# Optimization experiments

Measured on AMD Instinct MI355X. Metric: run time of the kernel, lower is better.

## Reference

```python
import jax, jax.numpy as jnp
import numpy as np

N_NODES = 100000


def gcn_conv(x, src, dst, W, b, n_nodes):
    """PyG-style GCNConv: linear transform, symmetric-normalized aggregation with self loops."""
    h = x @ W  # (N, out)
    e = src.shape[0]
    # degree including the implicit self loop (edge weights = 1)
    deg = jax.ops.segment_sum(jnp.ones((e,), dtype=h.dtype), dst, num_segments=n_nodes) + 1.0
    dis = jax.lax.rsqrt(deg)  # deg^{-1/2}
    coef = dis[src] * dis[dst]  # (E,)
    msg = h[src] * coef[:, None]  # (E, out) -- gather + scale
    agg = jax.ops.segment_sum(msg, dst, num_segments=n_nodes)  # scatter-add
    agg = agg + h * (dis * dis)[:, None]  # self-loop contribution
    return agg + b


def setup_inputs() -> dict:
    key = jax.random.key(0)
    k = jax.random.split(key, 6)
    in_dim, hid, out = 128, 128, 64
    E = 1600000
    x = jax.random.normal(k[0], (N_NODES, in_dim), dtype=jnp.float32)
    edge_index = jax.random.randint(k[1], (2, E), 0, N_NODES, dtype=jnp.int64)
    W1 = jax.random.normal(k[2], (in_dim, hid), dtype=jnp.float32) * (1.0 / np.sqrt(in_dim))
    b1 = jnp.zeros((hid,), dtype=jnp.float32)
    W2 = jax.random.normal(k[3], (hid, out), dtype=jnp.float32) * (1.0 / np.sqrt(hid))
    b2 = jnp.zeros((out,), dtype=jnp.float32)
    return {"x": x, "edge_index": edge_index, "W1": W1, "b1": b1, "W2": W2, "b2": b2}


def reference(x, edge_index, W1, b1, W2, b2):
    src, dst = edge_index[0], edge_index[1]
    h = gcn_conv(x, src, dst, W1, b1, N_NODES)
    h = jax.nn.relu(h)
    # dropout is identity in eval mode
    h = gcn_conv(h, src, dst, W2, b2, N_NODES)
    # L2 normalize along feature dim (F.normalize, eps=1e-12)
    norm = jnp.maximum(jnp.linalg.norm(h, axis=-1, keepdims=True), 1e-12)
    return h / norm
```

## Files before the change

### kernel.cpp

```cpp
#include <hip/hip_runtime.h>
#include <hip/hip_bf16.h>
#include <math.h>

#define CSHIFT 9
#define TILE   4096
#define PSH    14

using f16x8 = __attribute__((ext_vector_type(8))) _Float16;
using f16x2 = __attribute__((ext_vector_type(2))) _Float16;
using f32x4 = __attribute__((ext_vector_type(4))) float;

__device__ __forceinline__ unsigned pack_f16(float lo, float hi) {
    auto h = __builtin_amdgcn_cvt_pkrtz(lo, hi);
    return *(unsigned*)&h;
}
__device__ __forceinline__ f16x2 h2(unsigned u) { return *(f16x2*)&u; }

__device__ __forceinline__ unsigned pack_fp8x4(float f0, float f1, float f2, float f3) {
    int w = 0;
    w = __builtin_amdgcn_cvt_pk_fp8_f32(f0, f1, w, false);
    w = __builtin_amdgcn_cvt_pk_fp8_f32(f2, f3, w, true);
    return (unsigned)w;
}
__device__ __forceinline__ void fp8x4_acc(unsigned v, float& a0, float& a1, float& a2, float& a3) {
    auto lo = __builtin_amdgcn_cvt_pk_f32_fp8((int)v, false);
    auto hi = __builtin_amdgcn_cvt_pk_f32_fp8((int)v, true);
    a0 += lo[0]; a1 += lo[1]; a2 += hi[0]; a3 += hi[1];
}

__global__ void k_prep(const float* __restrict__ W1, const float* __restrict__ W2,
                       unsigned short* __restrict__ wp1, unsigned short* __restrict__ wp2,
                       int* __restrict__ ccursor, unsigned* __restrict__ g1,
                       unsigned* __restrict__ g2, int NC, int N) {
    int idx = blockIdx.x * 256 + threadIdx.x;
    if (idx < NC) ccursor[idx] = idx << PSH;
    if (idx < 32) {
        g1[(size_t)N * 32 + idx] = 0u;
        g2[(size_t)N * 32 + idx] = 0u;
    }
    if (idx < 16384) {
        int e = idx & 7, l = (idx >> 3) & 63, f = idx >> 9;
        int nt = f & 7, kt = f >> 3;
        int k = kt * 32 + (l >> 4) * 8 + e, nn = nt * 16 + (l & 15);
        _Float16 hv = (_Float16)W1[k * 128 + nn];
        wp1[idx] = *(unsigned short*)&hv;
    }
    int i2 = idx - 16384;
    if (i2 >= 0 && i2 < 8192) {
        int e = i2 & 7, l = (i2 >> 3) & 63, f = i2 >> 9;
        int nt = f & 3, kt = f >> 2;
        int k = kt * 32 + (l >> 4) * 8 + e, nn = nt * 16 + (l & 15);
        _Float16 hv = (_Float16)W2[k * 64 + nn];
        wp2[i2] = *(unsigned short*)&hv;
    }
}

__global__ __launch_bounds__(256) void k_part(const int* __restrict__ src,
                                              const int* __restrict__ dst, int E,
                                              int* __restrict__ ccursor,
                                              int* __restrict__ pairs, int NC) {
    __shared__ int sdst[TILE];
    __shared__ int stg[TILE];
    __shared__ unsigned char sbk[TILE];
    __shared__ int h[256], delta[256], cur[256];
    __shared__ int sa[256], sb[256];
    int t = threadIdx.x;
    int base = blockIdx.x * TILE;
    int cnt = min(TILE, E - base);

    h[t] = 0; __syncthreads();
    #pragma unroll
    for (int k = 0; k < TILE / 256; ++k) {
        int e = base + k * 256 + t;
        int d = (e < E) ? dst[e] : -1;
        sdst[k * 256 + t] = d;
        if (d >= 0) atomicAdd(&h[d >> CSHIFT], 1);
    }
    __syncthreads();
    int myc = h[t];
    int* c_ = sa; int* n_ = sb;
    c_[t] = myc; __syncthreads();
    for (int o = 1; o < 256; o <<= 1) {
        int val = c_[t] + ((t >= o) ? c_[t - o] : 0);
        n_[t] = val; __syncthreads();
        int* tmp = c_; c_ = n_; n_ = tmp;
    }
    int ex = c_[t] - myc;
    cur[t] = ex;
    int g = 0;
    if (t < NC && myc) g = atomicAdd(&ccursor[t], myc);
    delta[t] = g - ex;
    __syncthreads();

    #pragma unroll
    for (int k = 0; k < TILE / 256; ++k) {
        int e = base + k * 256 + t;
        if (e < E) {
            int d = sdst[k * 256 + t];
            int b = d >> CSHIFT;
            int p = atomicAdd(&cur[b], 1);
            stg[p] = src[e] | ((d & 511) << 17);
            sbk[p] = (unsigned char)b;
        }
    }
    __syncthreads();
    for (int i = t; i < cnt; i += 256)
        pairs[delta[sbk[i]] + i] = stg[i];
}

__global__ __launch_bounds__(256) void k_build(const int* __restrict__ ccursor,
                                               const int* __restrict__ pairs,
                                               int2* __restrict__ seg,
                                               float* __restrict__ dis,
                                               int* __restrict__ csr, int N) {
    __shared__ int h[512];
    __shared__ int cur[512];
    __shared__ int sa[256], sb[256];
    int b = blockIdx.x, t = threadIdx.x;
    h[t] = 0; h[t + 256] = 0; __syncthreads();
    int beg = b << PSH, end = ccursor[b];
    for (int i = beg + t; i < end; i += 256) atomicAdd(&h[pairs[i] >> 17], 1);
    __syncthreads();
    int h0 = h[2 * t], h1 = h[2 * t + 1];
    int p0 = (h0 + 15) & ~15;
    int p1 = (h1 + 15) & ~15;
    int s = p0 + p1;
    int* c_ = sa; int* n_ = sb;
    c_[t] = s; __syncthreads();
    for (int o = 1; o < 256; o <<= 1) {
        int val = c_[t] + ((t >= o) ? c_[t - o] : 0);
        n_[t] = val; __syncthreads();
        int* tmp = c_; c_ = n_; n_ = tmp;
    }
    int ex = c_[t] - s;
    int d0 = b << CSHIFT;
    int da = d0 + 2 * t, db = da + 1;
    cur[2 * t] = ex; cur[2 * t + 1] = ex + p0;
    if (da < N) { seg[da] = make_int2(beg + ex, beg + ex + p0);       dis[da] = rsqrtf((float)h0 + 1.0f); }
    if (db < N) { seg[db] = make_int2(beg + ex + p0, beg + ex + p0 + p1); dis[db] = rsqrtf((float)h1 + 1.0f); }
    for (int i = h0; i < p0; ++i) csr[beg + ex + i] = N;
    for (int i = h1; i < p1; ++i) csr[beg + ex + p0 + i] = N;
    __syncthreads();
    for (int i = beg + t; i < end; i += 256) {
        int pk = pairs[i];
        int p = atomicAdd(&cur[pk >> 17], 1);
        csr[beg + p] = pk & 0x1FFFF;
    }
}

__global__ __launch_bounds__(256) void k_gemm1(
    const float* __restrict__ A, const unsigned short* __restrict__ wp,
    const float* __restrict__ dis, unsigned* __restrict__ G, int M)
{
    constexpr int NT = 8;
    constexpr int ND = 32;

    union UW { uint4 q; f16x8 v; };
    union UA { unsigned u[4]; f16x8 v; };

    const int tid  = threadIdx.x;
    const int wv   = tid >> 6;
    const int lane = tid & 63;
    const int lm   = lane & 15;
    const int lk   = lane >> 4;
    const int m0   = blockIdx.x * 128 + wv * 32;

    f16x8 xf[2][4];
    int mrow[2];
    #pragma unroll
    for (int mt = 0; mt < 2; ++mt) {
        int m = m0 + mt * 16 + lm;
        mrow[mt] = m;
        int mc = m < M ? m : (M - 1);
        const float* Ar = A + (size_t)mc * 128;
        #pragma unroll
        for (int kt = 0; kt < 4; ++kt) {
            int cb = kt * 32 + lk * 8;
            float4 p = *(const float4*)(Ar + cb);
            float4 q = *(const float4*)(Ar + cb + 4);
            UA u;
            u.u[0] = pack_f16(p.x, p.y);
            u.u[1] = pack_f16(p.z, p.w);
            u.u[2] = pack_f16(q.x, q.y);
            u.u[3] = pack_f16(q.z, q.w);
            xf[mt][kt] = u.v;
        }
    }

    f32x4 acc[2][NT];
    #pragma unroll
    for (int mt = 0; mt < 2; ++mt)
        #pragma unroll
        for (int nt = 0; nt < NT; ++nt)
            #pragma unroll
            for (int r = 0; r < 4; ++r) acc[mt][nt][r] = 0.f;

    const uint4* wpv = (const uint4*)wp;
    #pragma unroll
    for (int kt = 0; kt < 4; ++kt) {
        f16x8 wf[NT];
        #pragma unroll
        for (int nt = 0; nt < NT; ++nt) {
            UW u; u.q = wpv[(kt * NT + nt) * 64 + lane];
            wf[nt] = u.v;
        }
        #pragma unroll
        for (int mt = 0; mt < 2; ++mt)
            #pragma unroll
            for (int nt = 0; nt < NT; ++nt)
                acc[mt][nt] = __builtin_amdgcn_mfma_f32_16x16x32_f16(
                    wf[nt], xf[mt][kt], acc[mt][nt], 0, 0, 0);
    }

    #pragma unroll
    for (int mt = 0; mt < 2; ++mt) {
        int m = mrow[mt];
        if (m < M) {
            float dd = dis[m];
            unsigned* gr = G + (size_t)m * ND;
            #pragma unroll
            for (int nt = 0; nt < NT; ++nt)
                gr[nt * 4 + lk] = pack_fp8x4(acc[mt][nt][0] * dd, acc[mt][nt][1] * dd,
                                             acc[mt][nt][2] * dd, acc[mt][nt][3] * dd);
        }
    }
}

__global__ __launch_bounds__(256) void k_agg1(
    const unsigned* __restrict__ g1, const int2* __restrict__ seg,
    const int* __restrict__ csr, const float* __restrict__ dis,
    const float* __restrict__ b1, unsigned* __restrict__ y1, int n)
{
    int wid  = (blockIdx.x * 256 + threadIdx.x) >> 6;
    int lane = threadIdx.x & 63;
    if (wid >= n) return;
    int d  = wid;
    int ll = lane & 31;
    int eh = lane >> 5;
    int2 se = seg[d];
    int beg = se.x, pend = se.y;

    float a0 = 0.f, a1 = 0.f, a2 = 0.f, a3 = 0.f;
    if (eh == 0)
        fp8x4_acc(g1[(size_t)d * 32 + ll], a0, a1, a2, a3);

    for (int j = beg; j < pend; j += 16) {
        unsigned v[8];
        #pragma unroll
        for (int k = 0; k < 8; ++k)
            v[k] = g1[(size_t)csr[j + 2 * k + eh] * 32 + ll];
        #pragma unroll
        for (int k = 0; k < 8; ++k)
            fp8x4_acc(v[k], a0, a1, a2, a3);
    }

    a0 += __shfl_xor(a0, 32, 64);
    a1 += __shfl_xor(a1, 32, 64);
    a2 += __shfl_xor(a2, 32, 64);
    a3 += __shfl_xor(a3, 32, 64);

    float dd = dis[d];
    float4 bb = *(const float4*)(b1 + 4 * ll);
    float o0 = fmaxf(fmaf(dd, a0, bb.x), 0.f);
    float o1 = fmaxf(fmaf(dd, a1, bb.y), 0.f);
    float o2 = fmaxf(fmaf(dd, a2, bb.z), 0.f);
    float o3 = fmaxf(fmaf(dd, a3, bb.w), 0.f);
    if (lane < 32) {
        uint2 w;
        w.x = pack_f16(o0, o1);
        w.y = pack_f16(o2, o3);
        *((uint2*)(y1 + (size_t)d * 64) + ll) = w;
    }
}

__global__ __launch_bounds__(256) void k_gemm2(
    const unsigned short* __restrict__ A, const unsigned short* __restrict__ wp,
    const float* __restrict__ dis, unsigned* __restrict__ G, int M)
{
    constexpr int NT = 4;
    constexpr int ND = 32;
    union UW { uint4 q; f16x8 v; };

    const int tid  = threadIdx.x;
    const int wv   = tid >> 6;
    const int lane = tid & 63;
    const int lm   = lane & 15;
    const int lk   = lane >> 4;
    const int m0   = blockIdx.x * 128 + wv * 32;

    f16x8 xf[2][4];
    int mrow[2];
    #pragma unroll
    for (int mt = 0; mt < 2; ++mt) {
        int m = m0 + mt * 16 + lm;
        mrow[mt] = m;
        int mc = m < M ? m : (M - 1);
        const uint4* Ar = (const uint4*)(A + (size_t)mc * 128);
        #pragma unroll
        for (int kt = 0; kt < 4; ++kt) {
            UW u; u.q = Ar[kt * 4 + lk];
            xf[mt][kt] = u.v;
        }
    }

    f32x4 acc[2][NT];
    #pragma unroll
    for (int mt = 0; mt < 2; ++mt)
        #pragma unroll
        for (int nt = 0; nt < NT; ++nt)
            #pragma unroll
            for (int r = 0; r < 4; ++r) acc[mt][nt][r] = 0.f;

    const uint4* wpv = (const uint4*)wp;
    #pragma unroll
    for (int kt = 0; kt < 4; ++kt) {
        f16x8 wf[NT];
        #pragma unroll
        for (int nt = 0; nt < NT; ++nt) {
            UW u; u.q = wpv[(kt * NT + nt) * 64 + lane];
            wf[nt] = u.v;
        }
        #pragma unroll
        for (int mt = 0; mt < 2; ++mt)
            #pragma unroll
            for (int nt = 0; nt < NT; ++nt)
                acc[mt][nt] = __builtin_amdgcn_mfma_f32_16x16x32_f16(
                    wf[nt], xf[mt][kt], acc[mt][nt], 0, 0, 0);
    }

    #pragma unroll
    for (int mt = 0; mt < 2; ++mt) {
        int m = mrow[mt];
        if (m < M) {
            float dd = dis[m];
            unsigned* gr = G + (size_t)m * ND;
            #pragma unroll
            for (int nt = 0; nt < NT; ++nt) {
                uint2 w;
                w.x = pack_f16(acc[mt][nt][0] * dd, acc[mt][nt][1] * dd);
                w.y = pack_f16(acc[mt][nt][2] * dd, acc[mt][nt][3] * dd);
                *(uint2*)(gr + nt * 8 + lk * 2) = w;
            }
        }
    }
}

__global__ __launch_bounds__(256) void k_agg2(
    const unsigned* __restrict__ g2, const int2* __restrict__ seg,
    const int* __restrict__ csr, const float* __restrict__ dis,
    const float* __restrict__ b2, float* __restrict__ out, int n)
{
    int wid  = (blockIdx.x * 256 + threadIdx.x) >> 6;
    int lane = threadIdx.x & 63;
    if (wid >= n) return;
    int d  = wid;
    int ql = lane & 15;
    int qh = lane >> 4;
    int2 se = seg[d];
    int beg = se.x, pend = se.y;

    float a0 = 0.f, a1 = 0.f, a2 = 0.f, a3 = 0.f;
    int j = beg;
    for (; j + 32 <= pend; j += 32) {
        uint2 v[8];
        #pragma unroll
        for (int k = 0; k < 8; ++k) {
            int s = csr[j + 4 * k + qh];
            v[k] = *((const uint2*)(g2 + (size_t)s * 32) + ql);
        }
        #pragma unroll
        for (int k = 0; k < 8; k += 2) {
            f16x2 sx = h2(v[k].x) + h2(v[k + 1].x);
            f16x2 sy = h2(v[k].y) + h2(v[k + 1].y);
            a0 += (float)sx[0]; a1 += (float)sx[1];
            a2 += (float)sy[0]; a3 += (float)sy[1];
        }
    }
    if (j < pend) {
        uint2 v[4];
        #pragma unroll
        for (int k = 0; k < 4; ++k) {
            int s = csr[j + 4 * k + qh];
            v[k] = *((const uint2*)(g2 + (size_t)s * 32) + ql);
        }
        #pragma unroll
        for (int k = 0; k < 4; k += 2) {
            f16x2 sx = h2(v[k].x) + h2(v[k + 1].x);
            f16x2 sy = h2(v[k].y) + h2(v[k + 1].y);
            a0 += (float)sx[0]; a1 += (float)sx[1];
            a2 += (float)sy[0]; a3 += (float)sy[1];
        }
    }

    a0 += __shfl_xor(a0, 16, 64); a0 += __shfl_xor(a0, 32, 64);
    a1 += __shfl_xor(a1, 16, 64); a1 += __shfl_xor(a1, 32, 64);
    a2 += __shfl_xor(a2, 16, 64); a2 += __shfl_xor(a2, 32, 64);
    a3 += __shfl_xor(a3, 16, 64); a3 += __shfl_xor(a3, 32, 64);

    uint2 sv = *((const uint2*)(g2 + (size_t)d * 32) + ql);
    f16x2 sx = h2(sv.x), sy = h2(sv.y);
    a0 += (float)sx[0]; a1 += (float)sx[1];
    a2 += (float)sy[0]; a3 += (float)sy[1];

    float dd = dis[d];
    float4 bb = *(const float4*)(b2 + 4 * ql);
    float v0 = fmaf(dd, a0, bb.x);
    float v1 = fmaf(dd, a1, bb.y);
    float v2 = fmaf(dd, a2, bb.z);
    float v3 = fmaf(dd, a3, bb.w);

    float ss = v0 * v0 + v1 * v1 + v2 * v2 + v3 * v3;
    #pragma unroll
    for (int o = 8; o >= 1; o >>= 1)
        ss += __shfl_xor(ss, o, 64);
    float inv = 1.0f / fmaxf(sqrtf(ss), 1e-12f);
    if (lane < 16) {
        float4 w = make_float4(v0 * inv, v1 * inv, v2 * inv, v3 * inv);
        *((float4*)(out + (size_t)d * 64) + ql) = w;
    }
}

extern "C" void kernel_launch(void* const* d_in, const int* in_sizes, int n_in,
                              void* d_out, int out_size, void* d_ws, size_t ws_size,
                              hipStream_t stream) {
    const float* x  = (const float*)d_in[0];
    const int*   ei = (const int*)d_in[1];
    const float* W1 = (const float*)d_in[2];
    const float* b1 = (const float*)d_in[3];
    const float* W2 = (const float*)d_in[4];
    const float* b2 = (const float*)d_in[5];

    const int N = in_sizes[0] / 128;
    const int E = in_sizes[1] / 2;
    const int* src = ei;
    const int* dst = ei + E;
    const int NC = (N + 511) >> CSHIFT;
    const int PB = (E + TILE - 1) / TILE;

    char* ws = (char*)d_ws;
    size_t cur = 0;
    auto alloc = [&](size_t bytes) -> void* {
        void* p = ws + cur;
        cur += (bytes + 255) & ~(size_t)255;
        return p;
    };
    int2*           seg     = (int2*)           alloc((size_t)N * 8);
    int*            ccursor = (int*)            alloc((size_t)NC * 4);
    float*          dis     = (float*)          alloc((size_t)N * 4);
    int*            csr     = (int*)            alloc(((size_t)NC << PSH) * 4);
    int*            pairs   = (int*)            alloc(((size_t)NC << PSH) * 4);
    unsigned short* wp1     = (unsigned short*) alloc(16384 * 2);
    unsigned short* wp2     = (unsigned short*) alloc(8192 * 2);
    unsigned*       g1      = (unsigned*)       alloc((size_t)(N + 1) * 32 * 4);
    unsigned*       y1      = (unsigned*)       alloc((size_t)N * 64 * 4);
    unsigned*       g2      = (unsigned*)       alloc((size_t)(N + 1) * 32 * 4);
    float*          out     = (float*)d_out;

    k_prep<<<96, 256, 0, stream>>>(W1, W2, wp1, wp2, ccursor, g1, g2, NC, N);
    k_part<<<PB, 256, 0, stream>>>(src, dst, E, ccursor, pairs, NC);
    k_build<<<NC, 256, 0, stream>>>(ccursor, pairs, seg, dis, csr, N);

    k_gemm1<<<(N + 127) / 128, 256, 0, stream>>>(x, wp1, dis, g1, N);
    k_agg1<<<(N * 64 + 255) / 256, 256, 0, stream>>>(g1, seg, csr, dis, b1, y1, N);
    k_gemm2<<<(N + 127) / 128, 256, 0, stream>>>((const unsigned short*)y1, wp2, dis, g2, N);
    k_agg2<<<(N * 64 + 255) / 256, 256, 0, stream>>>(g2, seg, csr, dis, b2, out, N);
}
```

Before: 165.1 us.

## Fold weight prep into partition kernel and widen aggregation gather loads

The separate prep kernel is removed: the weight packing and zero-row init now run in extra blocks of the partition kernel, and the cursor init becomes a memset with the bucket base offset added at use sites. Both aggregation kernels now have each lane gather a wider slice of the row (8 bytes of fp8 in agg1, 16 bytes of fp16 in agg2), so more edges are in flight per wave iteration, at the cost of extra shuffle reductions. The aim is to cut one launch and reduce the number of gather instructions per edge.

```diff
diff --git a/kernel.cpp b/kernel.cpp
--- a/kernel.cpp
+++ b/kernel.cpp
@@ -5,6 +5,7 @@
 #define CSHIFT 9
 #define TILE   4096
 #define PSH    14
+#define PREPB  96
 
 using f16x8 = __attribute__((ext_vector_type(8))) _Float16;
 using f16x2 = __attribute__((ext_vector_type(2))) _Float16;
@@ -28,37 +29,36 @@
     a0 += lo[0]; a1 += lo[1]; a2 += hi[0]; a3 += hi[1];
 }
 
-__global__ void k_prep(const float* __restrict__ W1, const float* __restrict__ W2,
-                       unsigned short* __restrict__ wp1, unsigned short* __restrict__ wp2,
-                       int* __restrict__ ccursor, unsigned* __restrict__ g1,
-                       unsigned* __restrict__ g2, int NC, int N) {
-    int idx = blockIdx.x * 256 + threadIdx.x;
-    if (idx < NC) ccursor[idx] = idx << PSH;
-    if (idx < 32) {
-        g1[(size_t)N * 32 + idx] = 0u;
-        g2[(size_t)N * 32 + idx] = 0u;
-    }
-    if (idx < 16384) {
-        int e = idx & 7, l = (idx >> 3) & 63, f = idx >> 9;
-        int nt = f & 7, kt = f >> 3;
-        int k = kt * 32 + (l >> 4) * 8 + e, nn = nt * 16 + (l & 15);
-        _Float16 hv = (_Float16)W1[k * 128 + nn];
-        wp1[idx] = *(unsigned short*)&hv;
-    }
-    int i2 = idx - 16384;
-    if (i2 >= 0 && i2 < 8192) {
-        int e = i2 & 7, l = (i2 >> 3) & 63, f = i2 >> 9;
-        int nt = f & 3, kt = f >> 2;
-        int k = kt * 32 + (l >> 4) * 8 + e, nn = nt * 16 + (l & 15);
-        _Float16 hv = (_Float16)W2[k * 64 + nn];
-        wp2[i2] = *(unsigned short*)&hv;
-    }
-}
-
-__global__ __launch_bounds__(256) void k_part(const int* __restrict__ src,
-                                              const int* __restrict__ dst, int E,
-                                              int* __restrict__ ccursor,
-                                              int* __restrict__ pairs, int NC) {
+__global__ __launch_bounds__(256) void k_part(
+    const int* __restrict__ src, const int* __restrict__ dst, int E,
+    int* __restrict__ ccursor, int* __restrict__ pairs, int NC, int PB,
+    const float* __restrict__ W1, const float* __restrict__ W2,
+    unsigned short* __restrict__ wp1, unsigned short* __restrict__ wp2,
+    unsigned* __restrict__ g1, unsigned* __restrict__ g2, int N)
+{
+    if ((int)blockIdx.x >= PB) {
+        int idx = (blockIdx.x - PB) * 256 + threadIdx.x;
+        if (idx < 32) {
+            g1[(size_t)N * 32 + idx] = 0u;
+            g2[(size_t)N * 32 + idx] = 0u;
+        }
+        if (idx < 16384) {
+            int e = idx & 7, l = (idx >> 3) & 63, f = idx >> 9;
+            int nt = f & 7, kt = f >> 3;
+            int k = kt * 32 + (l >> 4) * 8 + e, nn = nt * 16 + (l & 15);
+            _Float16 hv = (_Float16)W1[k * 128 + nn];
+            wp1[idx] = *(unsigned short*)&hv;
+        }
+        int i2 = idx - 16384;
+        if (i2 >= 0 && i2 < 8192) {
+            int e = i2 & 7, l = (i2 >> 3) & 63, f = i2 >> 9;
+            int nt = f & 3, kt = f >> 2;
+            int k = kt * 32 + (l >> 4) * 8 + e, nn = nt * 16 + (l & 15);
+            _Float16 hv = (_Float16)W2[k * 64 + nn];
+            wp2[i2] = *(unsigned short*)&hv;
+        }
+        return;
+    }
     __shared__ int sdst[TILE];
     __shared__ int stg[TILE];
     __shared__ unsigned char sbk[TILE];
@@ -89,7 +89,7 @@
     cur[t] = ex;
     int g = 0;
     if (t < NC && myc) g = atomicAdd(&ccursor[t], myc);
-    delta[t] = g - ex;
+    delta[t] = (t << PSH) + g - ex;
     __syncthreads();
 
     #pragma unroll
@@ -118,7 +118,7 @@
     __shared__ int sa[256], sb[256];
     int b = blockIdx.x, t = threadIdx.x;
     h[t] = 0; h[t + 256] = 0; __syncthreads();
-    int beg = b << PSH, end = ccursor[b];
+    int beg = b << PSH, end = beg + ccursor[b];
     for (int i = beg + t; i < end; i += 256) atomicAdd(&h[pairs[i] >> 17], 1);
     __syncthreads();
     int h0 = h[2 * t], h1 = h[2 * t + 1];
@@ -136,7 +136,7 @@
     int d0 = b << CSHIFT;
     int da = d0 + 2 * t, db = da + 1;
     cur[2 * t] = ex; cur[2 * t + 1] = ex + p0;
-    if (da < N) { seg[da] = make_int2(beg + ex, beg + ex + p0);       dis[da] = rsqrtf((float)h0 + 1.0f); }
+    if (da < N) { seg[da] = make_int2(beg + ex, beg + ex + p0);           dis[da] = rsqrtf((float)h0 + 1.0f); }
     if (db < N) { seg[db] = make_int2(beg + ex + p0, beg + ex + p0 + p1); dis[db] = rsqrtf((float)h1 + 1.0f); }
     for (int i = h0; i < p0; ++i) csr[beg + ex + i] = N;
     for (int i = h1; i < p1; ++i) csr[beg + ex + p0 + i] = N;
@@ -235,41 +235,74 @@
     int lane = threadIdx.x & 63;
     if (wid >= n) return;
     int d  = wid;
-    int ll = lane & 31;
-    int eh = lane >> 5;
+    int ql = lane & 15;
+    int qh = lane >> 4;
     int2 se = seg[d];
     int beg = se.x, pend = se.y;
 
     float a0 = 0.f, a1 = 0.f, a2 = 0.f, a3 = 0.f;
-    if (eh == 0)
-        fp8x4_acc(g1[(size_t)d * 32 + ll], a0, a1, a2, a3);
-
-    for (int j = beg; j < pend; j += 16) {
-        unsigned v[8];
-        #pragma unroll
-        for (int k = 0; k < 8; ++k)
-            v[k] = g1[(size_t)csr[j + 2 * k + eh] * 32 + ll];
-        #pragma unroll
-        for (int k = 0; k < 8; ++k)
-            fp8x4_acc(v[k], a0, a1, a2, a3);
-    }
-
-    a0 += __shfl_xor(a0, 32, 64);
-    a1 += __shfl_xor(a1, 32, 64);
-    a2 += __shfl_xor(a2, 32, 64);
-    a3 += __shfl_xor(a3, 32, 64);
-
-    float dd = dis[d];
-    float4 bb = *(const float4*)(b1 + 4 * ll);
-    float o0 = fmaxf(fmaf(dd, a0, bb.x), 0.f);
-    float o1 = fmaxf(fmaf(dd, a1, bb.y), 0.f);
-    float o2 = fmaxf(fmaf(dd, a2, bb.z), 0.f);
-    float o3 = fmaxf(fmaf(dd, a3, bb.w), 0.f);
-    if (lane < 32) {
-        uint2 w;
+    float a4 = 0.f, a5 = 0.f, a6 = 0.f, a7 = 0.f;
+    if (qh == 0) {
+        uint2 sv = *((const uint2*)(g1 + (size_t)d * 32) + ql);
+        fp8x4_acc(sv.x, a0, a1, a2, a3);
+        fp8x4_acc(sv.y, a4, a5, a6, a7);
+    }
+
+    int j = beg;
+    for (; j + 32 <= pend; j += 32) {
+        uint2 v[8];
+        #pragma unroll
+        for (int k = 0; k < 8; ++k) {
+            int s = csr[j + 4 * k + qh];
+            v[k] = *((const uint2*)(g1 + (size_t)s * 32) + ql);
+        }
+        #pragma unroll
+        for (int k = 0; k < 8; ++k) {
+            fp8x4_acc(v[k].x, a0, a1, a2, a3);
+            fp8x4_acc(v[k].y, a4, a5, a6, a7);
+        }
+    }
+    if (j < pend) {
+        uint2 v[4];
+        #pragma unroll
+        for (int k = 0; k < 4; ++k) {
+            int s = csr[j + 4 * k + qh];
+            v[k] = *((const uint2*)(g1 + (size_t)s * 32) + ql);
+        }
+        #pragma unroll
+        for (int k = 0; k < 4; ++k) {
+            fp8x4_acc(v[k].x, a0, a1, a2, a3);
+            fp8x4_acc(v[k].y, a4, a5, a6, a7);
+        }
+    }
+
+    a0 += __shfl_xor(a0, 16, 64); a0 += __shfl_xor(a0, 32, 64);
+    a1 += __shfl_xor(a1, 16, 64); a1 += __shfl_xor(a1, 32, 64);
+    a2 += __shfl_xor(a2, 16, 64); a2 += __shfl_xor(a2, 32, 64);
+    a3 += __shfl_xor(a3, 16, 64); a3 += __shfl_xor(a3, 32, 64);
+    a4 += __shfl_xor(a4, 16, 64); a4 += __shfl_xor(a4, 32, 64);
+    a5 += __shfl_xor(a5, 16, 64); a5 += __shfl_xor(a5, 32, 64);
+    a6 += __shfl_xor(a6, 16, 64); a6 += __shfl_xor(a6, 32, 64);
+    a7 += __shfl_xor(a7, 16, 64); a7 += __shfl_xor(a7, 32, 64);
+
+    if (qh == 0) {
+        float dd = dis[d];
+        float4 bb0 = *(const float4*)(b1 + 8 * ql);
+        float4 bb1 = *(const float4*)(b1 + 8 * ql + 4);
+        float o0 = fmaxf(fmaf(dd, a0, bb0.x), 0.f);
+        float o1 = fmaxf(fmaf(dd, a1, bb0.y), 0.f);
+        float o2 = fmaxf(fmaf(dd, a2, bb0.z), 0.f);
+        float o3 = fmaxf(fmaf(dd, a3, bb0.w), 0.f);
+        float o4 = fmaxf(fmaf(dd, a4, bb1.x), 0.f);
+        float o5 = fmaxf(fmaf(dd, a5, bb1.y), 0.f);
+        float o6 = fmaxf(fmaf(dd, a6, bb1.z), 0.f);
+        float o7 = fmaxf(fmaf(dd, a7, bb1.w), 0.f);
+        uint4 w;
         w.x = pack_f16(o0, o1);
         w.y = pack_f16(o2, o3);
-        *((uint2*)(y1 + (size_t)d * 64) + ll) = w;
+        w.z = pack_f16(o4, o5);
+        w.w = pack_f16(o6, o7);
+        *((uint4*)(y1 + (size_t)d * 64) + ql) = w;
     }
 }
 
@@ -354,69 +387,90 @@
     int lane = threadIdx.x & 63;
     if (wid >= n) return;
     int d  = wid;
-    int ql = lane & 15;
-    int qh = lane >> 4;
+    int ol = lane & 7;
+    int oh = lane >> 3;
     int2 se = seg[d];
     int beg = se.x, pend = se.y;
 
     float a0 = 0.f, a1 = 0.f, a2 = 0.f, a3 = 0.f;
+    float a4 = 0.f, a5 = 0.f, a6 = 0.f, a7 = 0.f;
+
     int j = beg;
     for (; j + 32 <= pend; j += 32) {
-        uint2 v[8];
-        #pragma unroll
-        for (int k = 0; k < 8; ++k) {
-            int s = csr[j + 4 * k + qh];
-            v[k] = *((const uint2*)(g2 + (size_t)s * 32) + ql);
-        }
-        #pragma unroll
-        for (int k = 0; k < 8; k += 2) {
-            f16x2 sx = h2(v[k].x) + h2(v[k + 1].x);
-            f16x2 sy = h2(v[k].y) + h2(v[k + 1].y);
-            a0 += (float)sx[0]; a1 += (float)sx[1];
-            a2 += (float)sy[0]; a3 += (float)sy[1];
+        uint4 v[4];
+        #pragma unroll
+        for (int k = 0; k < 4; ++k) {
+            int s = csr[j + 8 * k + oh];
+            v[k] = *((const uint4*)(g2 + (size_t)s * 32) + ol);
+        }
+        #pragma unroll
+        for (int k = 0; k < 4; k += 2) {
+            f16x2 s0 = h2(v[k].x) + h2(v[k + 1].x);
+            f16x2 s1 = h2(v[k].y) + h2(v[k + 1].y);
+            f16x2 s2 = h2(v[k].z) + h2(v[k + 1].z);
+            f16x2 s3 = h2(v[k].w) + h2(v[k + 1].w);
+            a0 += (float)s0[0]; a1 += (float)s0[1];
+            a2 += (float)s1[0]; a3 += (float)s1[1];
+            a4 += (float)s2[0]; a5 += (float)s2[1];
+            a6 += (float)s3[0]; a7 += (float)s3[1];
         }
     }
     if (j < pend) {
-        uint2 v[4];
-        #pragma unroll
-        for (int k = 0; k < 4; ++k) {
-            int s = csr[j + 4 * k + qh];
-            v[k] = *((const uint2*)(g2 + (size_t)s * 32) + ql);
-        }
-        #pragma unroll
-        for (int k = 0; k < 4; k += 2) {
-            f16x2 sx = h2(v[k].x) + h2(v[k + 1].x);
-            f16x2 sy = h2(v[k].y) + h2(v[k + 1].y);
-            a0 += (float)sx[0]; a1 += (float)sx[1];
-            a2 += (float)sy[0]; a3 += (float)sy[1];
-        }
-    }
-
-    a0 += __shfl_xor(a0, 16, 64); a0 += __shfl_xor(a0, 32, 64);
-    a1 += __shfl_xor(a1, 16, 64); a1 += __shfl_xor(a1, 32, 64);
-    a2 += __shfl_xor(a2, 16, 64); a2 += __shfl_xor(a2, 32, 64);
-    a3 += __shfl_xor(a3, 16, 64); a3 += __shfl_xor(a3, 32, 64);
-
-    uint2 sv = *((const uint2*)(g2 + (size_t)d * 32) + ql);
-    f16x2 sx = h2(sv.x), sy = h2(sv.y);
-    a0 += (float)sx[0]; a1 += (float)sx[1];
-    a2 += (float)sy[0]; a3 += (float)sy[1];
+        uint4 v[2];
+        #pragma unroll
+        for (int k = 0; k < 2; ++k) {
+            int s = csr[j + 8 * k + oh];
+            v[k] = *((const uint4*)(g2 + (size_t)s * 32) + ol);
+        }
+        f16x2 s0 = h2(v[0].x) + h2(v[1].x);
+        f16x2 s1 = h2(v[0].y) + h2(v[1].y);
+        f16x2 s2 = h2(v[0].z) + h2(v[1].z);
+        f16x2 s3 = h2(v[0].w) + h2(v[1].w);
+        a0 += (float)s0[0]; a1 += (float)s0[1];
+        a2 += (float)s1[0]; a3 += (float)s1[1];
+        a4 += (float)s2[0]; a5 += (float)s2[1];
+        a6 += (float)s3[0]; a7 += (float)s3[1];
+    }
+
+    a0 += __shfl_xor(a0, 8, 64); a0 += __shfl_xor(a0, 16, 64); a0 += __shfl_xor(a0, 32, 64);
+    a1 += __shfl_xor(a1, 8, 64); a1 += __shfl_xor(a1, 16, 64); a1 += __shfl_xor(a1, 32, 64);
+    a2 += __shfl_xor(a2, 8, 64); a2 += __shfl_xor(a2, 16, 64); a2 += __shfl_xor(a2, 32, 64);
+    a3 += __shfl_xor(a3, 8, 64); a3 += __shfl_xor(a3, 16, 64); a3 += __shfl_xor(a3, 32, 64);
+    a4 += __shfl_xor(a4, 8, 64); a4 += __shfl_xor(a4, 16, 64); a4 += __shfl_xor(a4, 32, 64);
+    a5 += __shfl_xor(a5, 8, 64); a5 += __shfl_xor(a5, 16, 64); a5 += __shfl_xor(a5, 32, 64);
+    a6 += __shfl_xor(a6, 8, 64); a6 += __shfl_xor(a6, 16, 64); a6 += __shfl_xor(a6, 32, 64);
+    a7 += __shfl_xor(a7, 8, 64); a7 += __shfl_xor(a7, 16, 64); a7 += __shfl_xor(a7, 32, 64);
+
+    uint4 sv = *((const uint4*)(g2 + (size_t)d * 32) + ol);
+    f16x2 sx0 = h2(sv.x), sx1 = h2(sv.y), sx2 = h2(sv.z), sx3 = h2(sv.w);
+    a0 += (float)sx0[0]; a1 += (float)sx0[1];
+    a2 += (float)sx1[0]; a3 += (float)sx1[1];
+    a4 += (float)sx2[0]; a5 += (float)sx2[1];
+    a6 += (float)sx3[0]; a7 += (float)sx3[1];
 
     float dd = dis[d];
-    float4 bb = *(const float4*)(b2 + 4 * ql);
-    float v0 = fmaf(dd, a0, bb.x);
-    float v1 = fmaf(dd, a1, bb.y);
-    float v2 = fmaf(dd, a2, bb.z);
-    float v3 = fmaf(dd, a3, bb.w);
-
-    float ss = v0 * v0 + v1 * v1 + v2 * v2 + v3 * v3;
-    #pragma unroll
-    for (int o = 8; o >= 1; o >>= 1)
-        ss += __shfl_xor(ss, o, 64);
+    float4 bb0 = *(const float4*)(b2 + 8 * ol);
+    float4 bb1 = *(const float4*)(b2 + 8 * ol + 4);
+    float v0 = fmaf(dd, a0, bb0.x);
+    float v1 = fmaf(dd, a1, bb0.y);
+    float v2 = fmaf(dd, a2, bb0.z);
+    float v3 = fmaf(dd, a3, bb0.w);
+    float v4 = fmaf(dd, a4, bb1.x);
+    float v5 = fmaf(dd, a5, bb1.y);
+    float v6 = fmaf(dd, a6, bb1.z);
+    float v7 = fmaf(dd, a7, bb1.w);
+
+    float ss = v0 * v0 + v1 * v1 + v2 * v2 + v3 * v3
+             + v4 * v4 + v5 * v5 + v6 * v6 + v7 * v7;
+    ss += __shfl_xor(ss, 1, 64);
+    ss += __shfl_xor(ss, 2, 64);
+    ss += __shfl_xor(ss, 4, 64);
     float inv = 1.0f / fmaxf(sqrtf(ss), 1e-12f);
-    if (lane < 16) {
-        float4 w = make_float4(v0 * inv, v1 * inv, v2 * inv, v3 * inv);
-        *((float4*)(out + (size_t)d * 64) + ql) = w;
+    if (oh == 0) {
+        float4 w0 = make_float4(v0 * inv, v1 * inv, v2 * inv, v3 * inv);
+        float4 w1 = make_float4(v4 * inv, v5 * inv, v6 * inv, v7 * inv);
+        *((float4*)(out + (size_t)d * 64 + 8 * ol))     = w0;
+        *((float4*)(out + (size_t)d * 64 + 8 * ol + 4)) = w1;
     }
 }
 
@@ -456,8 +510,9 @@
     unsigned*       g2      = (unsigned*)       alloc((size_t)(N + 1) * 32 * 4);
     float*          out     = (float*)d_out;
 
-    k_prep<<<96, 256, 0, stream>>>(W1, W2, wp1, wp2, ccursor, g1, g2, NC, N);
-    k_part<<<PB, 256, 0, stream>>>(src, dst, E, ccursor, pairs, NC);
+    hipMemsetAsync(ccursor, 0, (size_t)NC * 4, stream);
+    k_part<<<PB + PREPB, 256, 0, stream>>>(src, dst, E, ccursor, pairs, NC, PB,
+                                           W1, W2, wp1, wp2, g1, g2, N);
     k_build<<<NC, 256, 0, stream>>>(ccursor, pairs, seg, dis, csr, N);
 
     k_gemm1<<<(N + 127) / 128, 256, 0, stream>>>(x, wp1, dis, g1, N);
```

After: 165.3 us. About the same (+0.1%).
